# Kernel optimization log

Hardware: AMD Instinct MI355X
Metric: run time of the kernel (lower is better)

Reference implementation:

```python
import jax, jax.numpy as jnp
import numpy as np
import math

N, D = 8192, 64
KSIZE = 1.0


def setup_inputs() -> dict:
    key = jax.random.key(0)
    kx, kz = jax.random.split(key)
    X = jax.random.normal(kx, (N, D), dtype=jnp.float32)
    Z = jax.random.normal(kz, (N, D), dtype=jnp.float32)
    return {"X": X, "Z": Z}


def _kernel_mean(A, B, ksize):
    # squared pairwise distances via the Gram-matrix expansion instead of
    # materializing the [N, M, D] broadcast diff the torch code implies.
    a2 = jnp.sum(A * A, axis=-1)                      # [N]
    b2 = jnp.sum(B * B, axis=-1)                      # [M]
    d2 = a2[:, None] + b2[None, :] - 2.0 * (A @ B.T)  # [N, M]
    d2 = jnp.maximum(d2, 0.0)                         # numerical guard
    G = jnp.exp(-d2 / ksize) / math.sqrt(2.0 * math.pi * ksize)
    return jnp.mean(G)


def reference(X, Z):
    mxx = _kernel_mean(X, X, KSIZE)
    mzz = _kernel_mean(Z, Z, KSIZE)
    mxz = _kernel_mean(X, Z, KSIZE)
    return jnp.log(jnp.sqrt(mxx * mzz + 1e-5) / (mxz + 1e-5))
```

## Files before the change

kernel.cpp:

```cpp
#include <hip/hip_runtime.h>
#include <hip/hip_bf16.h>
#include <math.h>

#define NN 8192
#define DD 64
#define BI_MAX 64
#define BJ_MAX 128
#define TRI_N 4160
#define T1B TRI_N
#define T2B (2*TRI_N)
#define TILES_TOTAL 16512
#define TPB 16
#define NBLOCKS (TILES_TOTAL / TPB)
#define NSLOT 32
#define SLOT_STRIDE 16

#define PANEL_ELEMS 1024

typedef __bf16 bf16x8 __attribute__((ext_vector_type(8)));
typedef float f32x4 __attribute__((ext_vector_type(4)));

#if defined(__has_builtin)
#if __has_builtin(__builtin_amdgcn_exp2f)
#define EXP2F __builtin_amdgcn_exp2f
#endif
#endif
#ifndef EXP2F
#define EXP2F exp2f
#endif

#define FMAX3(a,b,c) fmaxf(fmaxf((a),(b)),(c))
#define FMAX4(a,b,c,d) fmaxf(FMAX3((a),(b),(c)),(d))


__global__ __launch_bounds__(256) void prep_kernel(
        const float* __restrict__ X, const float* __restrict__ Z,
        __hip_bfloat16* __restrict__ XbF, __hip_bfloat16* __restrict__ ZbF,
        float* __restrict__ na, float* __restrict__ nb,
        float* __restrict__ partial) {
    int tid = threadIdx.x;
    int gw = blockIdx.x * 4 + (tid >> 6);
    int lane = tid & 63;
    int lm = lane & 15, lk = lane >> 4;
    const float* src = (gw < 512) ? X : Z;
    __hip_bfloat16* dst = (gw < 512) ? XbF : ZbF;
    float* nrm = (gw < 512) ? na : nb;
    int p = (gw < 512) ? gw : gw - 512;
    int row = p * 16 + lm;

    float s = 0.f;
    #pragma unroll
    for (int ks = 0; ks < 2; ++ks) {
        const float4* q = (const float4*)(src + (size_t)row * DD + ks * 32 + lk * 8);
        float4 u = q[0], v = q[1];
        float w[8] = {u.x, u.y, u.z, u.w, v.x, v.y, v.z, v.w};
        unsigned int h[8];
        #pragma unroll
        for (int r = 0; r < 8; ++r) {
            __hip_bfloat16 b = __float2bfloat16(w[r]);
            h[r] = *(unsigned short*)&b;
            float xr = __bfloat162float(b);
            s = fmaf(xr, xr, s);
        }
        uint4 pk;
        pk.x = h[0] | (h[1] << 16); pk.y = h[2] | (h[3] << 16);
        pk.z = h[4] | (h[5] << 16); pk.w = h[6] | (h[7] << 16);
        *(uint4*)(dst + (size_t)p * PANEL_ELEMS + ks * 512 + lane * 8) = pk;
    }
    s += __shfl_xor(s, 16, 64);
    s += __shfl_xor(s, 32, 64);
    if (lk == 0) nrm[row] = -1.4426950408889634f * s;

    if (blockIdx.x == 0) {
        for (int i = tid; i < 3 * NSLOT * SLOT_STRIDE; i += 256) partial[i] = 0.f;
    }
}

__global__ __launch_bounds__(256, 3) void mmd_kernel(
        const __hip_bfloat16* __restrict__ XbFh, const __hip_bfloat16* __restrict__ ZbFh,
        const float* __restrict__ na, const float* __restrict__ nb,
        float* __restrict__ partial) {
    int tid = threadIdx.x;
    int wave = tid >> 6, lane = tid & 63;
    int wr = wave >> 1, wc = wave & 1;
    int lm = lane & 15;
    int lk = lane >> 4;
    __shared__ float wsum[4];
    const float C2 = 2.8853900817779268f;

    int t0 = blockIdx.x * TPB;
    int combo, bi, bj;
    if (t0 < T2B) {
        combo = (t0 < T1B) ? 0 : 1;
        int tt = t0 - (combo ? T1B : 0);
        int rr = (int)((129.0f - sqrtf(16641.0f - 4.0f * (float)tt)) * 0.5f);
        rr = rr < 0 ? 0 : (rr > 63 ? 63 : rr);
        while (rr > 0 && rr * (129 - rr) > tt) --rr;
        while ((rr + 1) * (128 - rr) <= tt) ++rr;
        bi = rr;
        bj = 2 * rr + (tt - rr * (129 - rr));
    } else {
        combo = 2;
        int rem = t0 - T2B;
        bi = rem >> 7;
        bj = rem & 127;
    }
    const bool sym = (combo != 2);
    const __bf16 *A, *B;
    const float *sa, *sb;
    const __bf16* XbF = (const __bf16*)XbFh;
    const __bf16* ZbF = (const __bf16*)ZbFh;
    if (combo == 0)      { A = XbF; B = XbF; sa = na; sb = na; }
    else if (combo == 1) { A = ZbF; B = ZbF; sa = nb; sb = nb; }
    else                 { A = XbF; B = ZbF; sa = na; sb = nb; }

    bf16x8 af[2][4];
    float nav[4][4], navrtmax[4], navmax;
    {
        int pA = bi * 8 + wr * 4;
        #pragma unroll
        for (int ks = 0; ks < 2; ++ks)
            #pragma unroll
            for (int rt = 0; rt < 4; ++rt)
                af[ks][rt] = *(const bf16x8*)(A + (size_t)(pA + rt) * PANEL_ELEMS + ks * 512 + lane * 8);
        int row0 = bi * 128 + wr * 64;
        #pragma unroll
        for (int rt = 0; rt < 4; ++rt) {
            #pragma unroll
            for (int r = 0; r < 4; ++r) nav[rt][r] = sa[row0 + rt * 16 + lk * 4 + r];
            navrtmax[rt] = FMAX4(nav[rt][0], nav[rt][1], nav[rt][2], nav[rt][3]);
        }
        navmax = FMAX4(navrtmax[0], navrtmax[1], navrtmax[2], navrtmax[3]);
    }

    bf16x8 bufB[2][2][2];
    float bufNb[2][2];
    {
        int pB = bj * 4 + wc * 2;
        #pragma unroll
        for (int ks = 0; ks < 2; ++ks)
            #pragma unroll
            for (int ct = 0; ct < 2; ++ct)
                bufB[0][ks][ct] = *(const bf16x8*)(B + (size_t)(pB + ct) * PANEL_ELEMS + ks * 512 + lane * 8);
        int col0 = bj * 64 + wc * 32;
        #pragma unroll
        for (int ct = 0; ct < 2; ++ct) bufNb[0][ct] = sb[col0 + ct * 16 + lm];
    }

    float lsum = 0.f;

    #pragma unroll
    for (int it = 0; it < TPB; ++it) {
        const int cur = it & 1, nxt = cur ^ 1;
        const bool last = (it + 1 == TPB);
        int row0 = bi * 128 + wr * 64;
        int col0 = bj * 64 + wc * 32;
        bool above = sym && (col0 >= row0 + 64);
        bool elemw = sym && !above;
        float tileScale = above ? 2.f : 1.f;

        int nbi = bi, nbj = bj;
        if (!last) {
            nbj = bj + 1;
            if (nbj == BJ_MAX) { nbi = bi + 1; nbj = sym ? 2 * nbi : 0; }
            int npB = nbj * 4 + wc * 2;
            #pragma unroll
            for (int ks = 0; ks < 2; ++ks)
                #pragma unroll
                for (int ct = 0; ct < 2; ++ct)
                    bufB[nxt][ks][ct] = *(const bf16x8*)(B + (size_t)(npB + ct) * PANEL_ELEMS + ks * 512 + lane * 8);
            int ncol0 = nbj * 64 + wc * 32;
            #pragma unroll
            for (int ct = 0; ct < 2; ++ct) bufNb[nxt][ct] = sb[ncol0 + ct * 16 + lm];
        }
        __builtin_amdgcn_sched_barrier(0);

        __builtin_amdgcn_s_setprio(1);
        f32x4 acc[4][2] = {};
        #pragma unroll
        for (int ks = 0; ks < 2; ++ks)
            #pragma unroll
            for (int rt = 0; rt < 4; ++rt)
                #pragma unroll
                for (int ct = 0; ct < 2; ++ct)
                    acc[rt][ct] = __builtin_amdgcn_mfma_f32_16x16x32_bf16(
                        af[ks][rt], bufB[cur][ks][ct], acc[rt][ct], 0, 0, 0);

        float m00 = FMAX4(acc[0][0][0], acc[0][0][1], acc[0][0][2], acc[0][0][3]);
        float m01 = FMAX4(acc[0][1][0], acc[0][1][1], acc[0][1][2], acc[0][1][3]);
        float m10 = FMAX4(acc[1][0][0], acc[1][0][1], acc[1][0][2], acc[1][0][3]);
        float m11 = FMAX4(acc[1][1][0], acc[1][1][1], acc[1][1][2], acc[1][1][3]);
        float m20 = FMAX4(acc[2][0][0], acc[2][0][1], acc[2][0][2], acc[2][0][3]);
        float m21 = FMAX4(acc[2][1][0], acc[2][1][1], acc[2][1][2], acc[2][1][3]);
        float m30 = FMAX4(acc[3][0][0], acc[3][0][1], acc[3][0][2], acc[3][0][3]);
        float m31 = FMAX4(acc[3][1][0], acc[3][1][1], acc[3][1][2], acc[3][1][3]);
        float gmax = fmaxf(FMAX4(m00, m01, m10, m11), FMAX4(m20, m21, m30, m31));
        __builtin_amdgcn_s_setprio(0);
        float nbmax = fmaxf(bufNb[cur][0], bufNb[cur][1]);
        float tileBound = fmaf(gmax, C2, navmax + nbmax);
        if (__any(tileBound > -30.f)) {
            #pragma unroll
            for (int rt = 0; rt < 4; ++rt) {
                #pragma unroll
                for (int ct = 0; ct < 2; ++ct) {
                    float fm = FMAX4(acc[rt][ct][0], acc[rt][ct][1], acc[rt][ct][2], acc[rt][ct][3]);
                    float fb = fmaf(fm, C2, navrtmax[rt] + bufNb[cur][ct]);
                    if (__any(fb > -30.f)) {
                        float base = bufNb[cur][ct];
                        float a0 = fmaf(acc[rt][ct][0], C2, nav[rt][0] + base);
                        float a1 = fmaf(acc[rt][ct][1], C2, nav[rt][1] + base);
                        float a2 = fmaf(acc[rt][ct][2], C2, nav[rt][2] + base);
                        float a3 = fmaf(acc[rt][ct][3], C2, nav[rt][3] + base);
                        float e0 = EXP2F(fminf(a0, 0.f));
                        float e1 = EXP2F(fminf(a1, 0.f));
                        float e2 = EXP2F(fminf(a2, 0.f));
                        float e3 = EXP2F(fminf(a3, 0.f));
                        if (elemw) {
                            int gcol = col0 + ct * 16 + lm;
                            int gr = row0 + rt * 16 + lk * 4;
                            e0 *= (gr + 0 < gcol) ? 2.f : ((gr + 0 == gcol) ? 1.f : 0.f);
                            e1 *= (gr + 1 < gcol) ? 2.f : ((gr + 1 == gcol) ? 1.f : 0.f);
                            e2 *= (gr + 2 < gcol) ? 2.f : ((gr + 2 == gcol) ? 1.f : 0.f);
                            e3 *= (gr + 3 < gcol) ? 2.f : ((gr + 3 == gcol) ? 1.f : 0.f);
                            lsum += (e0 + e1) + (e2 + e3);
                        } else {
                            lsum += tileScale * ((e0 + e1) + (e2 + e3));
                        }
                    }
                }
            }
        }

        if (!last && nbi != bi) {
            int npA = nbi * 8 + wr * 4;
            #pragma unroll
            for (int ks = 0; ks < 2; ++ks)
                #pragma unroll
                for (int rt = 0; rt < 4; ++rt)
                    af[ks][rt] = *(const bf16x8*)(A + (size_t)(npA + rt) * PANEL_ELEMS + ks * 512 + lane * 8);
            int nrow0 = nbi * 128 + wr * 64;
            #pragma unroll
            for (int rt = 0; rt < 4; ++rt) {
                #pragma unroll
                for (int r = 0; r < 4; ++r) nav[rt][r] = sa[nrow0 + rt * 16 + lk * 4 + r];
                navrtmax[rt] = FMAX4(nav[rt][0], nav[rt][1], nav[rt][2], nav[rt][3]);
            }
            navmax = FMAX4(navrtmax[0], navrtmax[1], navrtmax[2], navrtmax[3]);
            __builtin_amdgcn_sched_barrier(0);
        }
        bi = nbi; bj = nbj;
    }

    #pragma unroll
    for (int off = 32; off; off >>= 1) lsum += __shfl_xor(lsum, off, 64);
    if (lane == 0) wsum[wave] = lsum;
    __syncthreads();
    if (tid == 0) {
        float s = (wsum[0] + wsum[1]) + (wsum[2] + wsum[3]);
        int slot = combo * NSLOT + (blockIdx.x & (NSLOT - 1));
        atomicAdd(&partial[slot * SLOT_STRIDE], s);
    }
}

__global__ void final_kernel(const float* __restrict__ partial, float* __restrict__ out) {
    __shared__ float s3[3];
    int tid = threadIdx.x;
    if (tid < 3) s3[tid] = 0.f;
    __syncthreads();
    if (tid < 3 * NSLOT) {
        float v = partial[tid * SLOT_STRIDE];
        atomicAdd(&s3[tid / NSLOT], v);
    }
    __syncthreads();
    if (tid == 0) {
        double inv = 1.0 / ((double)NN * (double)NN * 2.5066282746310002);
        double mxx = (double)s3[0] * inv;
        double mzz = (double)s3[1] * inv;
        double mxz = (double)s3[2] * inv;
        double v = log(sqrt(mxx * mzz + 1e-5) / (mxz + 1e-5));
        out[0] = (float)v;
    }
}

extern "C" void kernel_launch(void* const* d_in, const int* in_sizes, int n_in,
                              void* d_out, int out_size, void* d_ws, size_t ws_size,
                              hipStream_t stream) {
    const float* X = (const float*)d_in[0];
    const float* Z = (const float*)d_in[1];
    char* ws = (char*)d_ws;
    __hip_bfloat16* XbF = (__hip_bfloat16*)(ws);
    __hip_bfloat16* ZbF = (__hip_bfloat16*)(ws + 1048576);
    float* na = (float*)(ws + 2097152);
    float* nb = (float*)(ws + 2097152 + 32768);
    float* partial = (float*)(ws + 2097152 + 65536);

    hipLaunchKernelGGL(prep_kernel, dim3(256), dim3(256), 0, stream,
                       X, Z, XbF, ZbF, na, nb, partial);
    hipLaunchKernelGGL(mmd_kernel, dim3(NBLOCKS), dim3(256), 0, stream, XbF, ZbF, na, nb, partial);
    hipLaunchKernelGGL(final_kernel, dim3(1), dim3(128), 0, stream, partial, (float*)d_out);
}
```

Before: 32.31 us.

## Reshape block tile to 256x32 with waves stacked along rows

Changes the per-block tile from 128x64 (2x2 waves) to 256x32, with all four waves stacked along rows and sharing the same 32 B columns. The triangular tile enumeration and the symmetric next-row start are recomputed for the new tile shape. Waves now share B loads but each loads a distinct A panel. The coarser diagonal granularity adds some wasted work in the symmetric combos (total tiles 16640 vs 16512).

```diff
diff --git a/kernel.cpp b/kernel.cpp
--- a/kernel.cpp
+++ b/kernel.cpp
@@ -4,12 +4,10 @@
 
 #define NN 8192
 #define DD 64
-#define BI_MAX 64
-#define BJ_MAX 128
-#define TRI_N 4160
-#define T1B TRI_N
-#define T2B (2*TRI_N)
-#define TILES_TOTAL 16512
+#define BJ_MAX 256
+#define T1B 4224
+#define T2B (2*T1B)
+#define TILES_TOTAL 16640
 #define TPB 16
 #define NBLOCKS (TILES_TOTAL / TPB)
 #define NSLOT 32
@@ -82,7 +80,6 @@
         float* __restrict__ partial) {
     int tid = threadIdx.x;
     int wave = tid >> 6, lane = tid & 63;
-    int wr = wave >> 1, wc = wave & 1;
     int lm = lane & 15;
     int lk = lane >> 4;
     __shared__ float wsum[4];
@@ -93,17 +90,17 @@
     if (t0 < T2B) {
         combo = (t0 < T1B) ? 0 : 1;
         int tt = t0 - (combo ? T1B : 0);
-        int rr = (int)((129.0f - sqrtf(16641.0f - 4.0f * (float)tt)) * 0.5f);
-        rr = rr < 0 ? 0 : (rr > 63 ? 63 : rr);
-        while (rr > 0 && rr * (129 - rr) > tt) --rr;
-        while ((rr + 1) * (128 - rr) <= tt) ++rr;
+        int rr = (int)((65.0f - sqrtf(4225.0f - (float)tt)) * 0.5f);
+        rr = rr < 0 ? 0 : (rr > 31 ? 31 : rr);
+        while (rr > 0 && 260 * rr - 4 * rr * rr > tt) --rr;
+        while (260 * (rr + 1) - 4 * (rr + 1) * (rr + 1) <= tt) ++rr;
         bi = rr;
-        bj = 2 * rr + (tt - rr * (129 - rr));
+        bj = 8 * rr + (tt - (260 * rr - 4 * rr * rr));
     } else {
         combo = 2;
         int rem = t0 - T2B;
-        bi = rem >> 7;
-        bj = rem & 127;
+        bi = rem >> 8;
+        bj = rem & 255;
     }
     const bool sym = (combo != 2);
     const __bf16 *A, *B;
@@ -117,13 +114,13 @@
     bf16x8 af[2][4];
     float nav[4][4], navrtmax[4], navmax;
     {
-        int pA = bi * 8 + wr * 4;
+        int pA = bi * 16 + wave * 4;
         #pragma unroll
         for (int ks = 0; ks < 2; ++ks)
             #pragma unroll
             for (int rt = 0; rt < 4; ++rt)
                 af[ks][rt] = *(const bf16x8*)(A + (size_t)(pA + rt) * PANEL_ELEMS + ks * 512 + lane * 8);
-        int row0 = bi * 128 + wr * 64;
+        int row0 = bi * 256 + wave * 64;
         #pragma unroll
         for (int rt = 0; rt < 4; ++rt) {
             #pragma unroll
@@ -136,13 +133,13 @@
     bf16x8 bufB[2][2][2];
     float bufNb[2][2];
     {
-        int pB = bj * 4 + wc * 2;
+        int pB = bj * 2;
         #pragma unroll
         for (int ks = 0; ks < 2; ++ks)
             #pragma unroll
             for (int ct = 0; ct < 2; ++ct)
                 bufB[0][ks][ct] = *(const bf16x8*)(B + (size_t)(pB + ct) * PANEL_ELEMS + ks * 512 + lane * 8);
-        int col0 = bj * 64 + wc * 32;
+        int col0 = bj * 32;
         #pragma unroll
         for (int ct = 0; ct < 2; ++ct) bufNb[0][ct] = sb[col0 + ct * 16 + lm];
     }
@@ -153,8 +150,8 @@
     for (int it = 0; it < TPB; ++it) {
         const int cur = it & 1, nxt = cur ^ 1;
         const bool last = (it + 1 == TPB);
-        int row0 = bi * 128 + wr * 64;
-        int col0 = bj * 64 + wc * 32;
+        int row0 = bi * 256 + wave * 64;
+        int col0 = bj * 32;
         bool above = sym && (col0 >= row0 + 64);
         bool elemw = sym && !above;
         float tileScale = above ? 2.f : 1.f;
@@ -162,14 +159,14 @@
         int nbi = bi, nbj = bj;
         if (!last) {
             nbj = bj + 1;
-            if (nbj == BJ_MAX) { nbi = bi + 1; nbj = sym ? 2 * nbi : 0; }
-            int npB = nbj * 4 + wc * 2;
+            if (nbj == BJ_MAX) { nbi = bi + 1; nbj = sym ? 8 * nbi : 0; }
+            int npB = nbj * 2;
             #pragma unroll
             for (int ks = 0; ks < 2; ++ks)
                 #pragma unroll
                 for (int ct = 0; ct < 2; ++ct)
                     bufB[nxt][ks][ct] = *(const bf16x8*)(B + (size_t)(npB + ct) * PANEL_ELEMS + ks * 512 + lane * 8);
-            int ncol0 = nbj * 64 + wc * 32;
+            int ncol0 = nbj * 32;
             #pragma unroll
             for (int ct = 0; ct < 2; ++ct) bufNb[nxt][ct] = sb[ncol0 + ct * 16 + lm];
         }
@@ -232,13 +229,13 @@
         }
 
         if (!last && nbi != bi) {
-            int npA = nbi * 8 + wr * 4;
+            int npA = nbi * 16 + wave * 4;
             #pragma unroll
             for (int ks = 0; ks < 2; ++ks)
                 #pragma unroll
                 for (int rt = 0; rt < 4; ++rt)
                     af[ks][rt] = *(const bf16x8*)(A + (size_t)(npA + rt) * PANEL_ELEMS + ks * 512 + lane * 8);
-            int nrow0 = nbi * 128 + wr * 64;
+            int nrow0 = nbi * 256 + wave * 64;
             #pragma unroll
             for (int rt = 0; rt < 4; ++rt) {
                 #pragma unroll
```

Measured after the change: 31.81 us. No clear change (-1.6%).
